# Performance work log

Measured on AMD Instinct MI355X. Metric: run time of the kernel, lower is better.

The kernel has to match this reference:

```python
import jax, jax.numpy as jnp
import numpy as np

N_NODES = 20000
N_EDGES = 640000
HID = 256
IN_F, IN_SIZE = 6, 6
OUT_F, FH = 6, 3
EDGE_DIM = 8
T_DIM, S_DIM = 4, 6
N_LAYERS = 5


def setup_inputs() -> dict:
    key = jax.random.key(0)
    ks = jax.random.split(key, 32)
    g = lambda i, shape, scale=0.05: jax.random.normal(ks[i], shape, dtype=jnp.float32) * scale
    inp = {
        "x": jax.random.normal(ks[0], (N_NODES, IN_F, IN_SIZE), dtype=jnp.float32),
        "edge_index": jax.random.randint(ks[1], (2, N_EDGES), 0, N_NODES, dtype=jnp.int32),
        "edge_attr": jax.random.normal(ks[2], (N_EDGES, EDGE_DIM), dtype=jnp.float32),
        "t": jax.random.normal(ks[3], (N_NODES, T_DIM), dtype=jnp.float32),
        "s": jax.random.normal(ks[4], (N_NODES, S_DIM), dtype=jnp.float32),
        # embedder
        "W_emb": g(5, (IN_F * IN_SIZE, HID)), "b_emb": jnp.zeros((HID,), jnp.float32),
        # spatio-temporal encoder: t/s linear embeds + fusion over concat(x, te, se)
        "W_t": g(6, (T_DIM, HID)), "b_t": jnp.zeros((HID,), jnp.float32),
        "W_s": g(7, (S_DIM, HID)), "b_s": jnp.zeros((HID,), jnp.float32),
        "W_f": g(8, (3 * HID, HID)), "b_f": jnp.zeros((HID,), jnp.float32),
        # layernorm
        "ln_g": jnp.ones((HID,), jnp.float32), "ln_b": jnp.zeros((HID,), jnp.float32),
        # 5 TransformerConv layers (heads=1): query/key/value/edge/skip linears
        "Wq": g(9, (N_LAYERS, HID, HID)), "bq": jnp.zeros((N_LAYERS, HID), jnp.float32),
        "Wk": g(10, (N_LAYERS, HID, HID)), "bk": jnp.zeros((N_LAYERS, HID), jnp.float32),
        "Wv": g(11, (N_LAYERS, HID, HID)), "bv": jnp.zeros((N_LAYERS, HID), jnp.float32),
        "We": g(12, (N_LAYERS, EDGE_DIM, HID)), "be": jnp.zeros((N_LAYERS, HID), jnp.float32),
        "Wskip": g(13, (N_LAYERS, HID, HID)), "bskip": jnp.zeros((N_LAYERS, HID), jnp.float32),
        # decoder
        "W_dec": g(14, (HID, OUT_F * FH)), "b_dec": jnp.zeros((OUT_F * FH,), jnp.float32),
    }
    return inp


def _layernorm(x, g, b, eps=1e-5):
    mu = jnp.mean(x, axis=-1, keepdims=True)
    var = jnp.mean((x - mu) ** 2, axis=-1, keepdims=True)
    return (x - mu) * jax.lax.rsqrt(var + eps) * g + b


def _transformer_conv(x, src, dst, edge_attr, Wq, bq, Wk, bk, Wv, bv, We, be, Wskip, bskip):
    n = x.shape[0]
    d = x.shape[1]
    q = x @ Wq + bq                      # [n, d]
    k = x @ Wk + bk
    v = x @ Wv + bv
    e = edge_attr @ We + be              # [E, d]
    kj = k[src] + e                      # gather + edge fuse [E, d]
    vj = v[src] + e
    alpha = jnp.sum(q[dst] * kj, axis=-1) / jnp.sqrt(jnp.float32(d))  # [E]
    # segment softmax over incoming edges of each destination node
    m = jax.ops.segment_max(alpha, dst, num_segments=n)
    a = jnp.exp(alpha - m[dst])
    denom = jax.ops.segment_sum(a, dst, num_segments=n)
    w = a / (denom[dst] + 1e-16)
    out = jax.ops.segment_sum(vj * w[:, None], dst, num_segments=n)  # [n, d]
    return out + x @ Wskip + bskip       # root/skip connection


def reference(x, edge_index, edge_attr, t, s,
              W_emb, b_emb, W_t, b_t, W_s, b_s, W_f, b_f, ln_g, ln_b,
              Wq, bq, Wk, bk, Wv, bv, We, be, Wskip, bskip, W_dec, b_dec):
    n = x.shape[0]
    h = x.reshape(n, -1) @ W_emb + b_emb
    te = t @ W_t + b_t
    se = s @ W_s + b_s
    h = jnp.concatenate([h, te, se], axis=-1) @ W_f + b_f   # spatio-temporal fuse
    h = jax.nn.relu(_layernorm(h, ln_g, ln_b))
    src, dst = edge_index[0], edge_index[1]
    for i in range(N_LAYERS):
        h = jax.nn.relu(_transformer_conv(h, src, dst, edge_attr,
                                          Wq[i], bq[i], Wk[i], bk[i], Wv[i], bv[i],
                                          We[i], be[i], Wskip[i], bskip[i]))
    out = h @ W_dec + b_dec
    return out.reshape(n, OUT_F, FH)
```

## Files before the change

kernel.cpp:

```cpp
#include <hip/hip_runtime.h>
#include <hip/hip_fp8.h>
#include <math.h>

#define NN 20000
#define NPAD 20096
#define NE 640000
#define NOUT 1152
#define GSS 272
#define KVB 512
#define CAP 80
#define RECB 32
#define SCQ 0.09016994f
#define ISCL 8.8057e-5f
#define TIDX(r,k) ((((r)>>4)*4096) + (((k)>>3)*128) + (((r)&15)*8) + ((k)&7))

typedef _Float16 f16;
typedef f16 f16x8 __attribute__((ext_vector_type(8)));
typedef f16 f16x4 __attribute__((ext_vector_type(4)));
typedef f16 h2    __attribute__((ext_vector_type(2)));
typedef float f32x4 __attribute__((ext_vector_type(4)));
typedef float f32x2 __attribute__((ext_vector_type(2)));

static __device__ __forceinline__ float fdot2(h2 a, h2 b, float c) {
#if __has_builtin(__builtin_amdgcn_fdot2)
  return __builtin_amdgcn_fdot2(a, b, c, false);
#else
  return c + (float)a[0]*(float)b[0] + (float)a[1]*(float)b[1];
#endif
}

static __device__ __forceinline__ float fast_exp2(float x) {
#if __has_builtin(__builtin_amdgcn_exp2f)
  return __builtin_amdgcn_exp2f(x);
#else
  return exp2f(x);
#endif
}

static __device__ __forceinline__ int sdot4(unsigned a, unsigned b, int c) {
#if __has_builtin(__builtin_amdgcn_sdot4)
  return __builtin_amdgcn_sdot4((int)a, (int)b, c, false);
#else
  int r = c;
  #pragma unroll
  for (int i = 0; i < 4; i++) {
    int ai = ((int)((a >> (8*i)) & 255) ^ 128) - 128;
    int bi = ((int)((b >> (8*i)) & 255) ^ 128) - 128;
    r += ai*bi;
  }
  return r;
#endif
}

static __device__ __forceinline__ unsigned pack_i8x4(float a, float b, float c, float d) {
  int i0 = (int)rintf(a), i1 = (int)rintf(b), i2 = (int)rintf(c), i3 = (int)rintf(d);
  i0 = max(-127, min(127, i0)); i1 = max(-127, min(127, i1));
  i2 = max(-127, min(127, i2)); i3 = max(-127, min(127, i3));
  return (unsigned)(i0 & 255) | ((unsigned)(i1 & 255) << 8)
       | ((unsigned)(i2 & 255) << 16) | ((unsigned)(i3 & 255) << 24);
}

static __device__ __forceinline__ unsigned pack_fp8x4(float a, float b, float c, float d) {
#if __has_builtin(__builtin_amdgcn_cvt_pk_fp8_f32)
  int r = __builtin_amdgcn_cvt_pk_fp8_f32(a, b, 0, false);
  r = __builtin_amdgcn_cvt_pk_fp8_f32(c, d, r, true);
  return (unsigned)r;
#else
  __hip_fp8_e4m3 w(a), x2(b), y(c), z(d);
  return (unsigned)w.__x | ((unsigned)x2.__x<<8) | ((unsigned)y.__x<<16) | ((unsigned)z.__x<<24);
#endif
}

template<bool HI>
static __device__ __forceinline__ f32x2 unpack_fp8x2(unsigned v) {
#if __has_builtin(__builtin_amdgcn_cvt_pk_f32_fp8)
  return __builtin_amdgcn_cvt_pk_f32_fp8((int)v, HI);
#else
  unsigned s = HI ? (v >> 16) : (v & 0xffff);
  __hip_fp8_e4m3 a, b; a.__x = (unsigned char)(s & 0xff); b.__x = (unsigned char)(s >> 8);
  return (f32x2){ (float)a, (float)b };
#endif
}

__global__ __launch_bounds__(256) void k_prep_all(
    const float* __restrict__ W_emb, const float* __restrict__ W_t,
    const float* __restrict__ W_s,   const float* __restrict__ W_f,
    const float* __restrict__ b_emb, const float* __restrict__ b_t,
    const float* __restrict__ b_s,   const float* __restrict__ b_f,
    const float* __restrict__ Wq, const float* __restrict__ Wk,
    const float* __restrict__ Wv, const float* __restrict__ Wsk,
    const float* __restrict__ We, const float* __restrict__ be,
    const float* __restrict__ bq, const float* __restrict__ bk,
    const float* __restrict__ bv, const float* __restrict__ bsk,
    f16* __restrict__ Wch, float* __restrict__ bc,
    f16* __restrict__ WT, float* __restrict__ b_all,
    f16* __restrict__ hA, f16* __restrict__ hB)
{
  __shared__ float smem[64*65];
  int b = blockIdx.x;
  int tid = threadIdx.x;

  if (b < 47) {
    int r = b, c = tid;
    if (r < 36) {
      float a = 0.f;
      for (int m = 0; m < 256; m++) a += W_emb[r*256+m] * W_f[m*256+c];
      Wch[r*256+c] = (f16)a;
    } else if (r < 40) {
      int rr = r - 36; float a = 0.f;
      for (int m = 0; m < 256; m++) a += W_t[rr*256+m] * W_f[(256+m)*256+c];
      Wch[r*256+c] = (f16)a;
    } else if (r < 46) {
      int rr = r - 40; float a = 0.f;
      for (int m = 0; m < 256; m++) a += W_s[rr*256+m] * W_f[(512+m)*256+c];
      Wch[r*256+c] = (f16)a;
    } else {
      float a = b_f[c];
      for (int m = 0; m < 256; m++) a += b_emb[m]*W_f[m*256+c];
      for (int m = 0; m < 256; m++) a += b_t[m]*W_f[(256+m)*256+c];
      for (int m = 0; m < 256; m++) a += b_s[m]*W_f[(512+m)*256+c];
      bc[c] = a;
    }
  } else if (b < 367) {
    float (*lds)[65] = (float(*)[65])smem;
    int bb = b - 47;
    int nt = bb & 3, kt = (bb >> 2) & 3, mat = (bb >> 4) & 3, L = bb >> 6;
    const float* src = (mat == 0 ? Wq : mat == 1 ? Wk : mat == 2 ? Wv : Wsk) + (size_t)L*65536;
    int k0 = kt*64, n0 = nt*64;
    int c = tid & 63, r4 = tid >> 6;
    #pragma unroll
    for (int rr = 0; rr < 16; rr++) {
      int row = rr*4 + r4;
      lds[row][c] = src[(size_t)(k0 + row)*256 + n0 + c];
    }
    __syncthreads();
    f16* dst = WT + (size_t)L*294912;
    int nl = tid & 63, kb2 = tid >> 6;
    int ng = mat*256 + n0 + nl;
    #pragma unroll
    for (int half = 0; half < 2; half++) {
      int kb = kb2 + half*4;
      f16x8 v;
      #pragma unroll
      for (int e = 0; e < 8; e++) v[e] = (f16)lds[kb*8 + e][nl];
      *(f16x8*)(dst + TIDX(ng, k0 + kb*8)) = v;
    }
  } else if (b < 412) {
    float* vec = smem;
    int bb = b - 367;
    int L = bb / 9;
    int t = bb % 9;
    vec[tid] = (t < 8) ? We[(size_t)L*2048 + t*256 + tid] : be[(size_t)L*256 + tid];
    __syncthreads();
    int wave = tid >> 6, lane = tid & 63;
    for (int k = wave; k < 256; k += 4) {
      f32x4 wq = *(const f32x4*)(Wq + (size_t)L*65536 + (size_t)k*256 + lane*4);
      f32x4 vv = *(const f32x4*)(vec + lane*4);
      float d = wq[0]*vv[0] + wq[1]*vv[1] + wq[2]*vv[2] + wq[3]*vv[3];
      #pragma unroll
      for (int o = 32; o; o >>= 1) d += __shfl_xor(d, o, 64);
      if (lane == 0) WT[(size_t)L*294912 + TIDX(1024 + t, k)] = (f16)d;
    }
  } else if (b < 417) {
    int L = b - 412;
    for (int c = tid; c < NOUT; c += 256) {
      float v;
      if (c < 256)       v = bq [L*256+c];
      else if (c < 512)  v = bk [L*256+(c-256)];
      else if (c < 768)  v = bv [L*256+(c-512)];
      else if (c < 1024) v = bsk[L*256+(c-768)];
      else if (c < 1032) {
        int t = c-1024; float a = 0.f;
        for (int m = 0; m < 256; m++) a += bq[L*256+m]*We[(size_t)L*2048 + t*256 + m];
        v = a;
      } else if (c == 1032) {
        float a = 0.f;
        for (int m = 0; m < 256; m++) a += bq[L*256+m]*be[L*256+m];
        v = a;
      } else v = 0.f;
      b_all[(size_t)L*NOUT + c] = v;
    }
  } else {
    f16* p = (b == 417 ? hA : hB) + (size_t)NN*256;
    f16x8 z = {};
    for (int i = tid; i < (NPAD-NN)*256/8; i += 256)
      *(f16x8*)(p + (size_t)i*8) = z;
  }
}

__global__ void k_scatter(const int* __restrict__ ei, const float* __restrict__ eattr,
                          int* cnt, char* __restrict__ rec)
{
  int e = blockIdx.x*256 + threadIdx.x;
  if (e < NE) {
    int d = ei[NE + e];
    int pos = atomicAdd(&cnt[d], 1);
    char* rp = rec + (size_t)(d*CAP + pos)*RECB;
    f32x4 a0 = *(const f32x4*)(eattr + (size_t)e*8);
    f32x4 a1 = *(const f32x4*)(eattr + (size_t)e*8 + 4);
    f16x8 ea = { (f16)a0[0],(f16)a0[1],(f16)a0[2],(f16)a0[3],
                 (f16)a1[0],(f16)a1[1],(f16)a1[2],(f16)a1[3] };
    *(f16x8*)rp = ea;
    *(int*)(rp + 16) = ei[e];
  }
}

__global__ __launch_bounds__(256) void k_encoder(
    const float* __restrict__ x, const float* __restrict__ t, const float* __restrict__ s,
    const f16* __restrict__ Wch, const float* __restrict__ bc,
    const float* __restrict__ lng, const float* __restrict__ lnb,
    f16* __restrict__ h)
{
  __shared__ f16 Wcs[46*256];
  __shared__ float xin[16][48];
  __shared__ float bcs[256], lgs[256], lbs[256];
  int tid = threadIdx.x;
  int u0 = blockIdx.x * 16;
  for (int i = tid; i < 46*128; i += 256)
    ((unsigned int*)Wcs)[i] = ((const unsigned int*)Wch)[i];
  bcs[tid] = bc[tid]; lgs[tid] = lng[tid]; lbs[tid] = lnb[tid];
  for (int i = tid; i < 576; i += 256) xin[i/36][i%36] = x[(size_t)u0*36 + i];
  if (tid < 64) xin[tid>>2][36 + (tid&3)] = t[(size_t)u0*4 + tid];
  if (tid < 96) xin[tid/6][40 + tid%6] = s[(size_t)u0*6 + tid];
  __syncthreads();
  int node = tid >> 4, cg = tid & 15;
  int u = u0 + node;
  float acc[16];
  #pragma unroll
  for (int j = 0; j < 16; j++) acc[j] = bcs[cg*16+j];
  for (int r = 0; r < 46; r++) {
    float xv = xin[node][r];
    const h2* wr = (const h2*)(Wcs + r*256 + cg*16);
    #pragma unroll
    for (int j2 = 0; j2 < 8; j2++) {
      h2 w2 = wr[j2];
      acc[j2*2]   += xv * (float)w2[0];
      acc[j2*2+1] += xv * (float)w2[1];
    }
  }
  float sm = 0.f, sq = 0.f;
  #pragma unroll
  for (int j = 0; j < 16; j++) { sm += acc[j]; sq += acc[j]*acc[j]; }
  #pragma unroll
  for (int o = 1; o < 16; o <<= 1) { sm += __shfl_xor(sm, o, 64); sq += __shfl_xor(sq, o, 64); }
  float mu  = sm * (1.f/256.f);
  float var = sq * (1.f/256.f) - mu*mu;
  float rin = rsqrtf(var + 1e-5f);
  f16x8 o0, o1;
  #pragma unroll
  for (int j = 0; j < 8; j++) {
    int c = cg*16 + j;
    float v = (acc[j]-mu)*rin*lgs[c] + lbs[c];
    o0[j] = (f16)fmaxf(v, 0.f);
  }
  #pragma unroll
  for (int j = 0; j < 8; j++) {
    int c = cg*16 + 8 + j;
    float v = (acc[8+j]-mu)*rin*lgs[c] + lbs[c];
    o1[j] = (f16)fmaxf(v, 0.f);
  }
  *(f16x8*)(h + TIDX(u, cg*16))   = o0;
  *(f16x8*)(h + TIDX(u, cg*16+8)) = o1;
}

__global__ __launch_bounds__(256) void k_gemm(
    const f16* __restrict__ A, const f16* __restrict__ BT,
    const float* __restrict__ bias,
    unsigned char* __restrict__ qt8, unsigned char* __restrict__ kvt,
    f16* __restrict__ gsk)
{
  const int NWG = (NPAD/128)*9;
  const int Q = NWG >> 3, R = NWG & 7;
  int bid = blockIdx.x;
  int xcd = bid & 7, jj = bid >> 3;
  int wg = (xcd < R ? xcd*(Q+1) : R*(Q+1) + (xcd-R)*Q) + jj;
  int bmt = wg / 9, bnt = wg - bmt*9;

  int tid = threadIdx.x;
  int wave = tid >> 6, lane = tid & 63;
  int wm = wave >> 1, wn = wave & 1;
  int bm = bmt*128 + wm*64;
  int bn = bnt*128 + wn*64;
  int lr = lane & 15;
  int kg = lane >> 4;
  f32x4 acc[4][4];
  #pragma unroll
  for (int i = 0; i < 4; i++)
    #pragma unroll
    for (int j = 0; j < 4; j++) acc[i][j] = (f32x4){0.f,0.f,0.f,0.f};

  const f16* Ab = A  + (size_t)(bm >> 4)*4096 + kg*128 + lr*8;
  const f16* Bb = BT + (size_t)(bn >> 4)*4096 + kg*128 + lr*8;

  f16x8 a0,a1,a2,a3,b0,b1,b2,b3;
  f16x8 c0,c1,c2,c3,d0,d1,d2,d3;

#define LDX(K0) \
  a0 = *(const f16x8*)(Ab + 0*4096 + (K0)*16); a1 = *(const f16x8*)(Ab + 1*4096 + (K0)*16); \
  a2 = *(const f16x8*)(Ab + 2*4096 + (K0)*16); a3 = *(const f16x8*)(Ab + 3*4096 + (K0)*16); \
  b0 = *(const f16x8*)(Bb + 0*4096 + (K0)*16); b1 = *(const f16x8*)(Bb + 1*4096 + (K0)*16); \
  b2 = *(const f16x8*)(Bb + 2*4096 + (K0)*16); b3 = *(const f16x8*)(Bb + 3*4096 + (K0)*16);
#define LDY(K0) \
  c0 = *(const f16x8*)(Ab + 0*4096 + (K0)*16); c1 = *(const f16x8*)(Ab + 1*4096 + (K0)*16); \
  c2 = *(const f16x8*)(Ab + 2*4096 + (K0)*16); c3 = *(const f16x8*)(Ab + 3*4096 + (K0)*16); \
  d0 = *(const f16x8*)(Bb + 0*4096 + (K0)*16); d1 = *(const f16x8*)(Bb + 1*4096 + (K0)*16); \
  d2 = *(const f16x8*)(Bb + 2*4096 + (K0)*16); d3 = *(const f16x8*)(Bb + 3*4096 + (K0)*16);
#define MMX() \
  acc[0][0]=__builtin_amdgcn_mfma_f32_16x16x32_f16(b0,a0,acc[0][0],0,0,0); \
  acc[0][1]=__builtin_amdgcn_mfma_f32_16x16x32_f16(b1,a0,acc[0][1],0,0,0); \
  acc[0][2]=__builtin_amdgcn_mfma_f32_16x16x32_f16(b2,a0,acc[0][2],0,0,0); \
  acc[0][3]=__builtin_amdgcn_mfma_f32_16x16x32_f16(b3,a0,acc[0][3],0,0,0); \
  acc[1][0]=__builtin_amdgcn_mfma_f32_16x16x32_f16(b0,a1,acc[1][0],0,0,0); \
  acc[1][1]=__builtin_amdgcn_mfma_f32_16x16x32_f16(b1,a1,acc[1][1],0,0,0); \
  acc[1][2]=__builtin_amdgcn_mfma_f32_16x16x32_f16(b2,a1,acc[1][2],0,0,0); \
  acc[1][3]=__builtin_amdgcn_mfma_f32_16x16x32_f16(b3,a1,acc[1][3],0,0,0); \
  acc[2][0]=__builtin_amdgcn_mfma_f32_16x16x32_f16(b0,a2,acc[2][0],0,0,0); \
  acc[2][1]=__builtin_amdgcn_mfma_f32_16x16x32_f16(b1,a2,acc[2][1],0,0,0); \
  acc[2][2]=__builtin_amdgcn_mfma_f32_16x16x32_f16(b2,a2,acc[2][2],0,0,0); \
  acc[2][3]=__builtin_amdgcn_mfma_f32_16x16x32_f16(b3,a2,acc[2][3],0,0,0); \
  acc[3][0]=__builtin_amdgcn_mfma_f32_16x16x32_f16(b0,a3,acc[3][0],0,0,0); \
  acc[3][1]=__builtin_amdgcn_mfma_f32_16x16x32_f16(b1,a3,acc[3][1],0,0,0); \
  acc[3][2]=__builtin_amdgcn_mfma_f32_16x16x32_f16(b2,a3,acc[3][2],0,0,0); \
  acc[3][3]=__builtin_amdgcn_mfma_f32_16x16x32_f16(b3,a3,acc[3][3],0,0,0);
#define MMY() \
  acc[0][0]=__builtin_amdgcn_mfma_f32_16x16x32_f16(d0,c0,acc[0][0],0,0,0); \
  acc[0][1]=__builtin_amdgcn_mfma_f32_16x16x32_f16(d1,c0,acc[0][1],0,0,0); \
  acc[0][2]=__builtin_amdgcn_mfma_f32_16x16x32_f16(d2,c0,acc[0][2],0,0,0); \
  acc[0][3]=__builtin_amdgcn_mfma_f32_16x16x32_f16(d3,c0,acc[0][3],0,0,0); \
  acc[1][0]=__builtin_amdgcn_mfma_f32_16x16x32_f16(d0,c1,acc[1][0],0,0,0); \
  acc[1][1]=__builtin_amdgcn_mfma_f32_16x16x32_f16(d1,c1,acc[1][1],0,0,0); \
  acc[1][2]=__builtin_amdgcn_mfma_f32_16x16x32_f16(d2,c1,acc[1][2],0,0,0); \
  acc[1][3]=__builtin_amdgcn_mfma_f32_16x16x32_f16(d3,c1,acc[1][3],0,0,0); \
  acc[2][0]=__builtin_amdgcn_mfma_f32_16x16x32_f16(d0,c2,acc[2][0],0,0,0); \
  acc[2][1]=__builtin_amdgcn_mfma_f32_16x16x32_f16(d1,c2,acc[2][1],0,0,0); \
  acc[2][2]=__builtin_amdgcn_mfma_f32_16x16x32_f16(d2,c2,acc[2][2],0,0,0); \
  acc[2][3]=__builtin_amdgcn_mfma_f32_16x16x32_f16(d3,c2,acc[2][3],0,0,0); \
  acc[3][0]=__builtin_amdgcn_mfma_f32_16x16x32_f16(d0,c3,acc[3][0],0,0,0); \
  acc[3][1]=__builtin_amdgcn_mfma_f32_16x16x32_f16(d1,c3,acc[3][1],0,0,0); \
  acc[3][2]=__builtin_amdgcn_mfma_f32_16x16x32_f16(d2,c3,acc[3][2],0,0,0); \
  acc[3][3]=__builtin_amdgcn_mfma_f32_16x16x32_f16(d3,c3,acc[3][3],0,0,0);

  LDX(0)
  LDY(32)
  MMX()
  LDX(64)
  MMY()
  LDY(96)
  MMX()
  LDX(128)
  MMY()
  LDY(160)
  MMX()
  LDX(192)
  MMY()
  LDY(224)
  MMX()
  MMY()
#undef LDX
#undef LDY
#undef MMX
#undef MMY

  #pragma unroll
  for (int j = 0; j < 4; j++) {
    int cb0 = bn + j*16;
    if (cb0 >= 1040) continue;
    int colq = cb0 + kg*4;
    f32x4 bv = *(const f32x4*)(bias + colq);
    #pragma unroll
    for (int i = 0; i < 4; i++) {
      int row = bm + i*16 + lr;
      float v0 = acc[i][j][0]+bv[0], v1 = acc[i][j][1]+bv[1];
      float v2 = acc[i][j][2]+bv[2], v3 = acc[i][j][3]+bv[3];
      if (cb0 < 256) {
        *(unsigned*)(qt8 + (size_t)row*256 + colq) = pack_i8x4(v0*32.f, v1*32.f, v2*32.f, v3*32.f);
      } else if (cb0 < 512) {
        *(unsigned*)(kvt + (size_t)row*KVB + (colq-256)) = pack_i8x4(v0*32.f, v1*32.f, v2*32.f, v3*32.f);
      } else if (cb0 < 768) {
        *(unsigned*)(kvt + (size_t)row*KVB + 256 + (colq-512)) = pack_fp8x4(v0, v1, v2, v3);
      } else if (cb0 < 1024) {
        f16x4 st = { (f16)v0, (f16)v1, (f16)v2, (f16)v3 };
        *(f16x4*)(gsk + (size_t)row*GSS + (colq-768)) = st;
      } else {
        f16x4 st = { (f16)(v0*SCQ), (f16)(v1*SCQ), (f16)(v2*SCQ), (f16)(v3*SCQ) };
        *(f16x4*)(gsk + (size_t)row*GSS + 256 + (colq-1024)) = st;
      }
    }
  }
}

__global__ __launch_bounds__(256) void k_attn(
    const unsigned char* __restrict__ qt8, const unsigned char* __restrict__ kvt,
    const f16* __restrict__ gsk, const char* __restrict__ rec,
    const float* __restrict__ WeL, const float* __restrict__ beL,
    const int* __restrict__ cnt, f16* __restrict__ hout)
{
  __shared__ int2 swls[4][CAP];
  int wid = threadIdx.x >> 6, lane = threadIdx.x & 63;
  int u = blockIdx.x*4 + wid;
  int deg = cnt[u];
  size_t ub = (size_t)u*CAP;

  {
    const uint4* qp = (const uint4*)(qt8 + (size_t)u*256);
    uint4 q[16];
    #pragma unroll
    for (int c = 0; c < 16; c++) q[c] = qp[c];
    const f16* gb = gsk + (size_t)u*GSS;
    f16x8 qe8 = *(const f16x8*)(gb + 256);
    float qbv = (float)gb[264];

    float ssum = 0.f;
    float ae[8];
    #pragma unroll
    for (int j = 0; j < 8; j++) ae[j] = 0.f;

    for (int i = lane; i < deg; i += 64) {
      const char* rp = rec + (ub + i)*RECB;
      f16x8 ea = *(const f16x8*)rp;
      int sn = *(const int*)(rp + 16);
      const uint4* kp = (const uint4*)(kvt + (size_t)sn*KVB);
      int di = 0;
      #pragma unroll
      for (int c = 0; c < 16; c++) {
        uint4 kw = kp[c];
        di = sdot4(kw.x, q[c].x, di);
        di = sdot4(kw.y, q[c].y, di);
        di = sdot4(kw.z, q[c].z, di);
        di = sdot4(kw.w, q[c].w, di);
      }
      float edot = 0.f;
      edot = fdot2((h2){ea[0],ea[1]}, (h2){qe8[0],qe8[1]}, edot);
      edot = fdot2((h2){ea[2],ea[3]}, (h2){qe8[2],qe8[3]}, edot);
      edot = fdot2((h2){ea[4],ea[5]}, (h2){qe8[4],qe8[5]}, edot);
      edot = fdot2((h2){ea[6],ea[7]}, (h2){qe8[6],qe8[7]}, edot);
      float w = fast_exp2((float)di*ISCL + edot + qbv);
      swls[wid][i] = make_int2(sn, __float_as_int(w));
      ssum += w;
      #pragma unroll
      for (int j = 0; j < 8; j++) ae[j] += w*(float)ea[j];
    }

    #pragma unroll
    for (int o = 1; o < 64; o <<= 1) {
      ssum += __shfl_xor(ssum, o, 64);
      #pragma unroll
      for (int j = 0; j < 8; j++) ae[j] += __shfl_xor(ae[j], o, 64);
    }

    int grp = lane >> 4;
    int gl  = lane & 15;
    float av[16];
    #pragma unroll
    for (int j = 0; j < 16; j++) av[j] = 0.f;

    #pragma unroll 2
    for (int i = grp; i < deg; i += 4) {
      int2 sw = swls[wid][i];
      float w = __int_as_float(sw.y);
      uint4 vw = *(const uint4*)(kvt + (size_t)sw.x*KVB + 256 + gl*16);
      f32x2 p;
      p = unpack_fp8x2<false>(vw.x); av[0]  += w*p[0]; av[1]  += w*p[1];
      p = unpack_fp8x2<true >(vw.x); av[2]  += w*p[0]; av[3]  += w*p[1];
      p = unpack_fp8x2<false>(vw.y); av[4]  += w*p[0]; av[5]  += w*p[1];
      p = unpack_fp8x2<true >(vw.y); av[6]  += w*p[0]; av[7]  += w*p[1];
      p = unpack_fp8x2<false>(vw.z); av[8]  += w*p[0]; av[9]  += w*p[1];
      p = unpack_fp8x2<true >(vw.z); av[10] += w*p[0]; av[11] += w*p[1];
      p = unpack_fp8x2<false>(vw.w); av[12] += w*p[0]; av[13] += w*p[1];
      p = unpack_fp8x2<true >(vw.w); av[14] += w*p[0]; av[15] += w*p[1];
    }

    #pragma unroll
    for (int j = 0; j < 16; j++) {
      av[j] += __shfl_xor(av[j], 16, 64);
      av[j] += __shfl_xor(av[j], 32, 64);
    }

    float inv = 1.f/(ssum + 1e-16f);
    int cb = gl*16 + grp*4;
    f16x4 sk = *(const f16x4*)(gsk + (size_t)u*GSS + cb);
    f16 res[4];
    #pragma unroll
    for (int t = 0; t < 4; t++) {
      int c = cb + t;
      float o = av[grp*4+t];
      o += ae[0]*WeL[0*256+c] + ae[1]*WeL[1*256+c] + ae[2]*WeL[2*256+c] + ae[3]*WeL[3*256+c];
      o += ae[4]*WeL[4*256+c] + ae[5]*WeL[5*256+c] + ae[6]*WeL[6*256+c] + ae[7]*WeL[7*256+c];
      o += ssum*beL[c];
      o = o*inv + (float)sk[t];
      res[t] = (f16)fmaxf(o, 0.f);
    }
    f16x4 outp = { res[0], res[1], res[2], res[3] };
    *(f16x4*)(hout + TIDX(u, cb)) = outp;
  }
}

__global__ __launch_bounds__(256) void k_decoder(
    const f16* __restrict__ h, const float* __restrict__ Wd,
    const float* __restrict__ bd, float* __restrict__ out)
{
  int n0 = blockIdx.x*32;
  __shared__ float hs[32*256];
  int tid = threadIdx.x;
  for (int j = tid; j < 32*32; j += 256) {
    int node = j >> 5, c8 = (j & 31)*8;
    f16x8 v = *(const f16x8*)(h + TIDX(n0 + node, c8));
    float* dst = &hs[node*256 + c8];
    #pragma unroll
    for (int e = 0; e < 8; e++) dst[e] = (float)v[e];
  }
  __syncthreads();
  for (int o = tid; o < 32*18; o += 256) {
    int ln = o/18, col = o - ln*18;
    int node = n0 + ln;
    float acc = bd[col];
    const float* hr = &hs[ln*256];
    #pragma unroll 4
    for (int k4 = 0; k4 < 64; k4++) {
      f32x4 hv = *(const f32x4*)(hr + k4*4);
      acc += hv[0]*Wd[(k4*4+0)*18+col] + hv[1]*Wd[(k4*4+1)*18+col]
           + hv[2]*Wd[(k4*4+2)*18+col] + hv[3]*Wd[(k4*4+3)*18+col];
    }
    out[(size_t)node*18 + col] = acc;
  }
}

extern "C" void kernel_launch(void* const* d_in, const int* in_sizes, int n_in,
                              void* d_out, int out_size, void* d_ws, size_t ws_size,
                              hipStream_t stream)
{
  const float* x     = (const float*)d_in[0];
  const int*   ei    = (const int*)  d_in[1];
  const float* eattr = (const float*)d_in[2];
  const float* t     = (const float*)d_in[3];
  const float* s     = (const float*)d_in[4];
  const float* W_emb = (const float*)d_in[5];
  const float* b_emb = (const float*)d_in[6];
  const float* W_t   = (const float*)d_in[7];
  const float* b_t   = (const float*)d_in[8];
  const float* W_s   = (const float*)d_in[9];
  const float* b_s   = (const float*)d_in[10];
  const float* W_f   = (const float*)d_in[11];
  const float* b_f   = (const float*)d_in[12];
  const float* ln_g  = (const float*)d_in[13];
  const float* ln_b  = (const float*)d_in[14];
  const float* Wq    = (const float*)d_in[15];
  const float* bq    = (const float*)d_in[16];
  const float* Wk    = (const float*)d_in[17];
  const float* bk    = (const float*)d_in[18];
  const float* Wv    = (const float*)d_in[19];
  const float* bv    = (const float*)d_in[20];
  const float* We    = (const float*)d_in[21];
  const float* be    = (const float*)d_in[22];
  const float* Wsk   = (const float*)d_in[23];
  const float* bsk   = (const float*)d_in[24];
  const float* W_dec = (const float*)d_in[25];
  const float* b_dec = (const float*)d_in[26];

  float* wsf = (float*)d_ws;
  size_t off = 0;
  float* bc    = wsf + off; off += 256;
  float* b_all = wsf + off; off += (size_t)5*NOUT;
  f16*   Wch   = (f16*)(wsf + off); off += (size_t)46*256/2;
  f16*   WT    = (f16*)(wsf + off); off += (size_t)5*294912/2;
  unsigned char* qt8 = (unsigned char*)(wsf + off); off += (size_t)NPAD*256/4;
  unsigned char* kvt = (unsigned char*)(wsf + off); off += (size_t)NPAD*KVB/4;
  f16*   gsk   = (f16*)(wsf + off); off += (size_t)NPAD*GSS/2;
  f16*   hA    = (f16*)(wsf + off); off += (size_t)NPAD*256/2;
  f16*   hB    = (f16*)(wsf + off); off += (size_t)NPAD*256/2;
  char*  rec   = (char*)(wsf + off); off += (size_t)NN*CAP*RECB/4;
  int*   cnt   = (int*)(wsf + off); off += NN;

  (void)hipMemsetAsync(cnt, 0, NN*sizeof(int), stream);
  k_prep_all<<<419, 256, 0, stream>>>(W_emb, W_t, W_s, W_f, b_emb, b_t, b_s, b_f,
                                      Wq, Wk, Wv, Wsk, We, be, bq, bk, bv, bsk,
                                      Wch, bc, WT, b_all, hA, hB);
  k_scatter <<<(NE+255)/256, 256, 0, stream>>>(ei, eattr, cnt, rec);

  k_encoder <<<NN/16, 256, 0, stream>>>(x, t, s, Wch, bc, ln_g, ln_b, hA);

  f16* hin = hA;
  f16* hot = hB;
  for (int L = 0; L < 5; L++) {
    k_gemm<<<(NPAD/128)*9, 256, 0, stream>>>(hin, WT + (size_t)L*294912,
                                             b_all + (size_t)L*NOUT, qt8, kvt, gsk);
    k_attn<<<NN/4, 256, 0, stream>>>(qt8, kvt, gsk, rec, We + (size_t)L*2048,
                                     be + (size_t)L*256, cnt, hot);
    f16* tmp = hin; hin = hot; hot = tmp;
  }
  k_decoder<<<NN/32, 256, 0, stream>>>(hin, W_dec, b_dec, (float*)d_out);
}
```

Before: 669.5 us.

## Split attention into separate alpha-score and value-aggregation kernels

Splits the per-node attention kernel into two launches. The first computes edge scores, writes each exp-weight back into the edge record, and stores per-node sums and edge-attribute aggregates to a stats buffer. The second reads those weights and accumulates the values. This removes the LDS staging and may lower register pressure and raise occupancy in each kernel, at the cost of an extra launch per layer and extra global traffic for the weights and stats.

```diff
diff --git a/kernel.cpp b/kernel.cpp
--- a/kernel.cpp
+++ b/kernel.cpp
@@ -389,110 +389,131 @@
   }
 }
 
-__global__ __launch_bounds__(256) void k_attn(
+__global__ __launch_bounds__(256) void k_alpha(
     const unsigned char* __restrict__ qt8, const unsigned char* __restrict__ kvt,
-    const f16* __restrict__ gsk, const char* __restrict__ rec,
+    const f16* __restrict__ gsk, char* __restrict__ rec,
+    const int* __restrict__ cnt, float* __restrict__ stats)
+{
+  int wid = threadIdx.x >> 6, lane = threadIdx.x & 63;
+  int u = __builtin_amdgcn_readfirstlane(blockIdx.x*4 + wid);
+  int deg = cnt[u];
+  const uint4* qp = (const uint4*)(qt8 + (size_t)u*256);
+  uint4 q[16];
+  #pragma unroll
+  for (int c = 0; c < 16; c++) q[c] = qp[c];
+  const f16* gb = gsk + (size_t)u*GSS;
+  f16x8 qe8 = *(const f16x8*)(gb + 256);
+  float qbv = (float)gb[264];
+  size_t ub = (size_t)u*CAP;
+
+  float ssum = 0.f;
+  float ae[8];
+  #pragma unroll
+  for (int j = 0; j < 8; j++) ae[j] = 0.f;
+
+  for (int i = lane; i < deg; i += 64) {
+    char* rp = rec + (ub + i)*RECB;
+    f16x8 ea = *(const f16x8*)rp;
+    int sn = *(const int*)(rp + 16);
+    const uint4* kp = (const uint4*)(kvt + (size_t)sn*KVB);
+    int di = 0;
+    #pragma unroll
+    for (int c = 0; c < 16; c++) {
+      uint4 kw = kp[c];
+      di = sdot4(kw.x, q[c].x, di);
+      di = sdot4(kw.y, q[c].y, di);
+      di = sdot4(kw.z, q[c].z, di);
+      di = sdot4(kw.w, q[c].w, di);
+    }
+    float edot = 0.f;
+    edot = fdot2((h2){ea[0],ea[1]}, (h2){qe8[0],qe8[1]}, edot);
+    edot = fdot2((h2){ea[2],ea[3]}, (h2){qe8[2],qe8[3]}, edot);
+    edot = fdot2((h2){ea[4],ea[5]}, (h2){qe8[4],qe8[5]}, edot);
+    edot = fdot2((h2){ea[6],ea[7]}, (h2){qe8[6],qe8[7]}, edot);
+    float w = fast_exp2((float)di*ISCL + edot + qbv);
+    *(float*)(rp + 20) = w;
+    ssum += w;
+    #pragma unroll
+    for (int j = 0; j < 8; j++) ae[j] += w*(float)ea[j];
+  }
+
+  #pragma unroll
+  for (int o = 1; o < 64; o <<= 1) {
+    ssum += __shfl_xor(ssum, o, 64);
+    #pragma unroll
+    for (int j = 0; j < 8; j++) ae[j] += __shfl_xor(ae[j], o, 64);
+  }
+  if (lane == 0) {
+    float* sp = stats + (size_t)u*12;
+    sp[0] = ssum;
+    *(f32x4*)(sp + 4) = (f32x4){ae[0], ae[1], ae[2], ae[3]};
+    *(f32x4*)(sp + 8) = (f32x4){ae[4], ae[5], ae[6], ae[7]};
+  }
+}
+
+__global__ __launch_bounds__(256) void k_attn2(
+    const unsigned char* __restrict__ kvt, const f16* __restrict__ gsk,
+    const char* __restrict__ rec,
     const float* __restrict__ WeL, const float* __restrict__ beL,
-    const int* __restrict__ cnt, f16* __restrict__ hout)
-{
-  __shared__ int2 swls[4][CAP];
-  int wid = threadIdx.x >> 6, lane = threadIdx.x & 63;
+    const int* __restrict__ cnt, const float* __restrict__ stats,
+    f16* __restrict__ hout)
+{
+  int wid  = threadIdx.x >> 6;
+  int lane = threadIdx.x & 63;
+  int grp  = lane >> 4;
+  int gl   = lane & 15;
   int u = blockIdx.x*4 + wid;
   int deg = cnt[u];
   size_t ub = (size_t)u*CAP;
 
-  {
-    const uint4* qp = (const uint4*)(qt8 + (size_t)u*256);
-    uint4 q[16];
-    #pragma unroll
-    for (int c = 0; c < 16; c++) q[c] = qp[c];
-    const f16* gb = gsk + (size_t)u*GSS;
-    f16x8 qe8 = *(const f16x8*)(gb + 256);
-    float qbv = (float)gb[264];
-
-    float ssum = 0.f;
-    float ae[8];
-    #pragma unroll
-    for (int j = 0; j < 8; j++) ae[j] = 0.f;
-
-    for (int i = lane; i < deg; i += 64) {
-      const char* rp = rec + (ub + i)*RECB;
-      f16x8 ea = *(const f16x8*)rp;
-      int sn = *(const int*)(rp + 16);
-      const uint4* kp = (const uint4*)(kvt + (size_t)sn*KVB);
-      int di = 0;
-      #pragma unroll
-      for (int c = 0; c < 16; c++) {
-        uint4 kw = kp[c];
-        di = sdot4(kw.x, q[c].x, di);
-        di = sdot4(kw.y, q[c].y, di);
-        di = sdot4(kw.z, q[c].z, di);
-        di = sdot4(kw.w, q[c].w, di);
-      }
-      float edot = 0.f;
-      edot = fdot2((h2){ea[0],ea[1]}, (h2){qe8[0],qe8[1]}, edot);
-      edot = fdot2((h2){ea[2],ea[3]}, (h2){qe8[2],qe8[3]}, edot);
-      edot = fdot2((h2){ea[4],ea[5]}, (h2){qe8[4],qe8[5]}, edot);
-      edot = fdot2((h2){ea[6],ea[7]}, (h2){qe8[6],qe8[7]}, edot);
-      float w = fast_exp2((float)di*ISCL + edot + qbv);
-      swls[wid][i] = make_int2(sn, __float_as_int(w));
-      ssum += w;
-      #pragma unroll
-      for (int j = 0; j < 8; j++) ae[j] += w*(float)ea[j];
-    }
-
-    #pragma unroll
-    for (int o = 1; o < 64; o <<= 1) {
-      ssum += __shfl_xor(ssum, o, 64);
-      #pragma unroll
-      for (int j = 0; j < 8; j++) ae[j] += __shfl_xor(ae[j], o, 64);
-    }
-
-    int grp = lane >> 4;
-    int gl  = lane & 15;
-    float av[16];
-    #pragma unroll
-    for (int j = 0; j < 16; j++) av[j] = 0.f;
-
-    #pragma unroll 2
-    for (int i = grp; i < deg; i += 4) {
-      int2 sw = swls[wid][i];
-      float w = __int_as_float(sw.y);
-      uint4 vw = *(const uint4*)(kvt + (size_t)sw.x*KVB + 256 + gl*16);
-      f32x2 p;
-      p = unpack_fp8x2<false>(vw.x); av[0]  += w*p[0]; av[1]  += w*p[1];
-      p = unpack_fp8x2<true >(vw.x); av[2]  += w*p[0]; av[3]  += w*p[1];
-      p = unpack_fp8x2<false>(vw.y); av[4]  += w*p[0]; av[5]  += w*p[1];
-      p = unpack_fp8x2<true >(vw.y); av[6]  += w*p[0]; av[7]  += w*p[1];
-      p = unpack_fp8x2<false>(vw.z); av[8]  += w*p[0]; av[9]  += w*p[1];
-      p = unpack_fp8x2<true >(vw.z); av[10] += w*p[0]; av[11] += w*p[1];
-      p = unpack_fp8x2<false>(vw.w); av[12] += w*p[0]; av[13] += w*p[1];
-      p = unpack_fp8x2<true >(vw.w); av[14] += w*p[0]; av[15] += w*p[1];
-    }
-
-    #pragma unroll
-    for (int j = 0; j < 16; j++) {
-      av[j] += __shfl_xor(av[j], 16, 64);
-      av[j] += __shfl_xor(av[j], 32, 64);
-    }
-
-    float inv = 1.f/(ssum + 1e-16f);
-    int cb = gl*16 + grp*4;
-    f16x4 sk = *(const f16x4*)(gsk + (size_t)u*GSS + cb);
-    f16 res[4];
-    #pragma unroll
-    for (int t = 0; t < 4; t++) {
-      int c = cb + t;
-      float o = av[grp*4+t];
-      o += ae[0]*WeL[0*256+c] + ae[1]*WeL[1*256+c] + ae[2]*WeL[2*256+c] + ae[3]*WeL[3*256+c];
-      o += ae[4]*WeL[4*256+c] + ae[5]*WeL[5*256+c] + ae[6]*WeL[6*256+c] + ae[7]*WeL[7*256+c];
-      o += ssum*beL[c];
-      o = o*inv + (float)sk[t];
-      res[t] = (f16)fmaxf(o, 0.f);
-    }
-    f16x4 outp = { res[0], res[1], res[2], res[3] };
-    *(f16x4*)(hout + TIDX(u, cb)) = outp;
-  }
+  float av[16];
+  #pragma unroll
+  for (int j = 0; j < 16; j++) av[j] = 0.f;
+
+  #pragma unroll 2
+  for (int i = grp; i < deg; i += 4) {
+    const char* rp = rec + (ub + i)*RECB;
+    int2 sw = *(const int2*)(rp + 16);
+    float w = __int_as_float(sw.y);
+    uint4 vw = *(const uint4*)(kvt + (size_t)sw.x*KVB + 256 + gl*16);
+    f32x2 p;
+    p = unpack_fp8x2<false>(vw.x); av[0]  += w*p[0]; av[1]  += w*p[1];
+    p = unpack_fp8x2<true >(vw.x); av[2]  += w*p[0]; av[3]  += w*p[1];
+    p = unpack_fp8x2<false>(vw.y); av[4]  += w*p[0]; av[5]  += w*p[1];
+    p = unpack_fp8x2<true >(vw.y); av[6]  += w*p[0]; av[7]  += w*p[1];
+    p = unpack_fp8x2<false>(vw.z); av[8]  += w*p[0]; av[9]  += w*p[1];
+    p = unpack_fp8x2<true >(vw.z); av[10] += w*p[0]; av[11] += w*p[1];
+    p = unpack_fp8x2<false>(vw.w); av[12] += w*p[0]; av[13] += w*p[1];
+    p = unpack_fp8x2<true >(vw.w); av[14] += w*p[0]; av[15] += w*p[1];
+  }
+
+  #pragma unroll
+  for (int j = 0; j < 16; j++) {
+    av[j] += __shfl_xor(av[j], 16, 64);
+    av[j] += __shfl_xor(av[j], 32, 64);
+  }
+
+  const float* sp = stats + (size_t)u*12;
+  float ssum = sp[0];
+  f32x4 aeA = *(const f32x4*)(sp + 4);
+  f32x4 aeB = *(const f32x4*)(sp + 8);
+  float inv = 1.f/(ssum + 1e-16f);
+
+  int cb = gl*16 + grp*4;
+  f16x4 sk = *(const f16x4*)(gsk + (size_t)u*GSS + cb);
+  f16 res[4];
+  #pragma unroll
+  for (int t = 0; t < 4; t++) {
+    int c = cb + t;
+    float o = av[grp*4+t];
+    o += aeA[0]*WeL[0*256+c] + aeA[1]*WeL[1*256+c] + aeA[2]*WeL[2*256+c] + aeA[3]*WeL[3*256+c];
+    o += aeB[0]*WeL[4*256+c] + aeB[1]*WeL[5*256+c] + aeB[2]*WeL[6*256+c] + aeB[3]*WeL[7*256+c];
+    o += ssum*beL[c];
+    o = o*inv + (float)sk[t];
+    res[t] = (f16)fmaxf(o, 0.f);
+  }
+  f16x4 outp = { res[0], res[1], res[2], res[3] };
+  *(f16x4*)(hout + TIDX(u, cb)) = outp;
 }
 
 __global__ __launch_bounds__(256) void k_decoder(
@@ -569,6 +590,7 @@
   f16*   hA    = (f16*)(wsf + off); off += (size_t)NPAD*256/2;
   f16*   hB    = (f16*)(wsf + off); off += (size_t)NPAD*256/2;
   char*  rec   = (char*)(wsf + off); off += (size_t)NN*CAP*RECB/4;
+  float* stats = wsf + off; off += (size_t)NN*12;
   int*   cnt   = (int*)(wsf + off); off += NN;
 
   (void)hipMemsetAsync(cnt, 0, NN*sizeof(int), stream);
@@ -584,8 +606,9 @@
   for (int L = 0; L < 5; L++) {
     k_gemm<<<(NPAD/128)*9, 256, 0, stream>>>(hin, WT + (size_t)L*294912,
                                              b_all + (size_t)L*NOUT, qt8, kvt, gsk);
-    k_attn<<<NN/4, 256, 0, stream>>>(qt8, kvt, gsk, rec, We + (size_t)L*2048,
-                                     be + (size_t)L*256, cnt, hot);
+    k_alpha<<<NN/4, 256, 0, stream>>>(qt8, kvt, gsk, rec, cnt, stats);
+    k_attn2<<<NN/4, 256, 0, stream>>>(kvt, gsk, rec, We + (size_t)L*2048,
+                                      be + (size_t)L*256, cnt, stats, hot);
     f16* tmp = hin; hin = hot; hot = tmp;
   }
   k_decoder<<<NN/32, 256, 0, stream>>>(hin, W_dec, b_dec, (float*)d_out);
```

After: 584.8 us. -12.7%, faster.
